# Optimization experiments

Hardware: AMD Instinct MI355X
Metric: run time of the kernel (lower is better)

## Reference

```python
import jax, jax.numpy as jnp
import numpy as np

B, S, D = 4, 2048, 1024
H = 2 * D          # hidden_dim = 2*n_embd
A = H // 16        # adapt_dim = 128
E = 8              # num_experts
K = 2              # top-k within group
GS = 4             # group_size
G = E // GS        # num_groups


def _ln(x, g, b, eps=1e-5):
    m = x.mean(-1, keepdims=True)
    v = x.var(-1, keepdims=True)
    return (x - m) / jnp.sqrt(v + eps) * g + b


def setup_inputs() -> dict:
    key = jax.random.key(0)
    ks = jax.random.split(key, 12)
    s = 1.0 / np.sqrt(D)       # shared MLP init scale
    sa = s * 0.01              # adapt layers init scale
    se = 0.01 / np.sqrt(A)     # expert adapter init scale
    f32 = jnp.float32
    return {
        "x": jax.random.normal(ks[0], (B, S, D), f32),
        "W_up": jax.random.normal(ks[1], (H, D), f32) * s,
        "W_gate": jax.random.normal(ks[2], (H, D), f32) * s,
        "W_down": jax.random.normal(ks[3], (D, H), f32) * s,
        "W_pre": jax.random.normal(ks[4], (A, D), f32) * sa,
        "W_post": jax.random.normal(ks[5], (A, H), f32) * sa,
        "g_an": jnp.ones((A,), f32),
        "b_an": jnp.zeros((A,), f32),
        "W_aproj": jax.random.normal(ks[6], (H, A), f32) * sa,
        "W_eadapt": jax.random.normal(ks[7], (E, A, A), f32) * se,
        "g_e": jnp.ones((E, A), f32),
        "b_e": jnp.zeros((E, A), f32),
        "W_eproj": jax.random.normal(ks[8], (H, A), f32) * se,
        "W_oproj": jax.random.normal(ks[9], (D, H), f32) * se,
        "W_rg": jax.random.normal(ks[10], (G, D), f32) * 0.001,
        "W_re": jax.random.normal(ks[11], (GS, D), f32) * 0.001,
    }


def reference(x, W_up, W_gate, W_down, W_pre, W_post, g_an, b_an, W_aproj,
              W_eadapt, g_e, b_e, W_eproj, W_oproj, W_rg, W_re):
    Bs, Ss, Ds = x.shape
    N = Bs * Ss
    xf = x.reshape(N, Ds)

    # ---- HierarchicalRouter ----
    gl = xf @ W_rg.T                                   # [N, G]
    gp = jax.nn.softmax(gl, axis=-1)
    gw = gp.max(axis=-1)                               # top-1 group weight
    gi = gp.argmax(axis=-1)                            # top-1 group index
    ll = xf @ W_re.T                                   # [N, GS]
    lp = jax.nn.softmax(ll, axis=-1)
    lw, li = jax.lax.top_k(lp, K)                      # [N, K]
    eidx = gi[:, None] * GS + li                       # global expert ids
    lw = lw / (lw.sum(-1, keepdims=True) + 1e-7)
    fw = gw[:, None] * lw                              # final weights [N, K]
    dispatch = jnp.zeros((N, E), x.dtype).at[jnp.arange(N)[:, None], eidx].set(fw)
    load = dispatch.sum(0)
    target = load.sum() / E
    load_balance_loss = jnp.mean((load - target) ** 2)
    z_loss = jnp.mean(gl ** 2) + jnp.mean(ll ** 2)
    router_loss = 0.001 * (load_balance_loss + z_loss)

    # ---- SharedExpertMLP ----
    up = x @ W_up.T                                    # [B, S, H]
    gate = x @ W_gate.T
    hidden = jax.nn.silu(gate) * up
    pre = x @ W_pre.T                                  # [B, S, A]
    a_in = _ln(pre, g_an, b_an)
    a_out = _ln(hidden @ W_post.T, g_an, b_an)
    aw = jax.nn.silu(jnp.clip(jnp.einsum('bsa,bta->bst', a_in, a_out), -5.0, 5.0))
    adapt = jnp.einsum('bst,bta->bsa', aw, a_in) @ W_aproj.T  # [B, S, H]
    hidden = hidden + 0.1 * adapt
    shared = hidden @ W_down.T                         # [B, S, D]

    # ---- ExpertGroup (vectorized gather/MLP/scatter) ----
    # sum_i w_i * (shared + 0.1*contrib_i) = shared*sum(w) + 0.1*sum_i w_i*contrib_i
    w = dispatch.reshape(Bs, Ss, E)                    # dispatch weights
    he = jnp.einsum('bsa,eca->ebsc', pre, W_eadapt)    # [E, B, S, A]
    he = _ln(he, g_e[:, None, None, :], b_e[:, None, None, :])
    wh = jnp.einsum('ebsa,bse->bsa', he, w)            # weighted combine at adapt_dim
    contrib = (wh @ W_eproj.T) @ W_oproj.T             # [B, S, D]
    out = shared * w.sum(-1, keepdims=True) + 0.1 * contrib
    return out, router_loss
```

## Files before the change

kernel.cpp:

```cpp
#include <hip/hip_runtime.h>
#include <hip/hip_bf16.h>

typedef unsigned short u16;
typedef short bf16x8 __attribute__((ext_vector_type(8)));
typedef float f32x4 __attribute__((ext_vector_type(4)));

#define N_TOK 8192
#define DIM   1024
#define HID   2048
#define ADIM  128
#define SEQ   2048
#define LDP   2304

__device__ __forceinline__ u16 f2bf_bits(float f){
  unsigned u = __float_as_uint(f);
  unsigned r = (u + 0x7fffu + ((u >> 16) & 1u)) >> 16;
  return (u16)r;
}
__device__ __forceinline__ float bf2f(u16 v){ return __uint_as_float((unsigned)v << 16); }
__device__ __forceinline__ float siluf(float x){ return x / (1.f + __expf(-x)); }

__device__ __forceinline__ void gload16(const void* g, void* l){
  __builtin_amdgcn_global_load_lds((const __attribute__((address_space(1))) void*)g,
                                   (__attribute__((address_space(3))) void*)l, 16, 0, 0);
}


__global__ void __launch_bounds__(512, 2)
gemm_gu256(const u16* __restrict__ X, const u16* __restrict__ Wgu,
           const float* __restrict__ sumw, u16* __restrict__ hidP)
{
  extern __shared__ u16 lds[];
  const int tid = threadIdx.x, w = tid >> 6, lane = tid & 63;
  const int wm = w >> 2, wn = w & 3;
  const int xcd = blockIdx.x & 7, lloc = blockIdx.x >> 3;
  const int bm = (xcd >> 1) * 8 + (lloc & 7);
  const int bn = (xcd & 1) * 8 + (lloc >> 3);
  const long brow = (long)bm * 256, bcol = (long)bn * 256;
  const int frow = lane & 15;
  const int fks = ((lane >> 4) * 8) ^ (((lane >> 1) & 3) << 3);
  const int srow = lane >> 2;
  const int sslot = (((lane & 3) ^ ((lane >> 3) & 3)) * 8);

  f32x4 acc[8][4];
  #pragma unroll
  for (int m = 0; m < 8; m++)
    #pragma unroll
    for (int n = 0; n < 4; n++)
      #pragma unroll
      for (int i = 0; i < 4; i++) acc[m][n][i] = 0.f;

  auto stage = [&](const u16* __restrict__ gbase, long row0, int kt, int kh,
                   int p, int regoff) {
    #pragma unroll
    for (int i = 0; i < 2; i++) {
      const int r = (i * 8 + w) * 16 + srow;
      const u16* g = gbase + (row0 + r) * 1024 + kt * 64 + kh * 32 + sslot;
      u16* l = &lds[p * 32768 + regoff + kh * 8192 + (i * 8 + w) * 512];
      gload16(g, l);
    }
  };

#define AFRAG(mf, kss) (*(const bf16x8*)&lds[p*32768 + (kss)*8192 + (wm*128 + (mf)*16 + frow)*32 + fks])
#define BFRAG(nf, kss) (*(const bf16x8*)&lds[p*32768 + 16384 + (kss)*8192 + (wn*64 + (nf)*16 + frow)*32 + fks])

  stage(X, brow, 0, 0, 0, 0);
  stage(Wgu, bcol, 0, 0, 0, 16384);
  stage(X, brow, 0, 1, 0, 0);
  stage(Wgu, bcol, 0, 1, 0, 16384);
  asm volatile("s_waitcnt vmcnt(4)" ::: "memory");
  __builtin_amdgcn_s_barrier();

  for (int kt = 0; kt < 16; ++kt) {
    const int p = kt & 1, pn = p ^ 1;
    const int ktn = (kt < 15) ? kt + 1 : 15;
    bf16x8 b[4], a[4];

    #pragma unroll
    for (int n = 0; n < 4; n++) b[n] = BFRAG(n, 0);
    #pragma unroll
    for (int m = 0; m < 4; m++) a[m] = AFRAG(m, 0);
    stage(X, brow, ktn, 0, pn, 0);
    __builtin_amdgcn_s_barrier();
    asm volatile("s_waitcnt lgkmcnt(0)" ::: "memory");
    __builtin_amdgcn_sched_barrier(0);
    __builtin_amdgcn_s_setprio(1);
    #pragma unroll
    for (int m = 0; m < 4; m++)
      #pragma unroll
      for (int n = 0; n < 4; n++)
        acc[m][n] = __builtin_amdgcn_mfma_f32_16x16x32_bf16(a[m], b[n], acc[m][n], 0, 0, 0);
    __builtin_amdgcn_s_setprio(0);
    __builtin_amdgcn_s_barrier();

    #pragma unroll
    for (int m = 0; m < 4; m++) a[m] = AFRAG(m + 4, 0);
    stage(Wgu, bcol, ktn, 0, pn, 16384);
    __builtin_amdgcn_s_barrier();
    asm volatile("s_waitcnt lgkmcnt(0)" ::: "memory");
    __builtin_amdgcn_sched_barrier(0);
    __builtin_amdgcn_s_setprio(1);
    #pragma unroll
    for (int m = 0; m < 4; m++)
      #pragma unroll
      for (int n = 0; n < 4; n++)
        acc[m + 4][n] = __builtin_amdgcn_mfma_f32_16x16x32_bf16(a[m], b[n], acc[m + 4][n], 0, 0, 0);
    __builtin_amdgcn_s_setprio(0);
    asm volatile("s_waitcnt vmcnt(4)" ::: "memory");
    __builtin_amdgcn_s_barrier();

    #pragma unroll
    for (int n = 0; n < 4; n++) b[n] = BFRAG(n, 1);
    #pragma unroll
    for (int m = 0; m < 4; m++) a[m] = AFRAG(m, 1);
    stage(X, brow, ktn, 1, pn, 0);
    __builtin_amdgcn_s_barrier();
    asm volatile("s_waitcnt lgkmcnt(0)" ::: "memory");
    __builtin_amdgcn_sched_barrier(0);
    __builtin_amdgcn_s_setprio(1);
    #pragma unroll
    for (int m = 0; m < 4; m++)
      #pragma unroll
      for (int n = 0; n < 4; n++)
        acc[m][n] = __builtin_amdgcn_mfma_f32_16x16x32_bf16(a[m], b[n], acc[m][n], 0, 0, 0);
    __builtin_amdgcn_s_setprio(0);
    __builtin_amdgcn_s_barrier();

    #pragma unroll
    for (int m = 0; m < 4; m++) a[m] = AFRAG(m + 4, 1);
    stage(Wgu, bcol, ktn, 1, pn, 16384);
    __builtin_amdgcn_s_barrier();
    asm volatile("s_waitcnt lgkmcnt(0)" ::: "memory");
    __builtin_amdgcn_sched_barrier(0);
    __builtin_amdgcn_s_setprio(1);
    #pragma unroll
    for (int m = 0; m < 4; m++)
      #pragma unroll
      for (int n = 0; n < 4; n++)
        acc[m + 4][n] = __builtin_amdgcn_mfma_f32_16x16x32_bf16(a[m], b[n], acc[m + 4][n], 0, 0, 0);
    __builtin_amdgcn_s_setprio(0);
    asm volatile("s_waitcnt vmcnt(4)" ::: "memory");
    __builtin_amdgcn_s_barrier();
  }
#undef AFRAG
#undef BFRAG

  #pragma unroll
  for (int mf = 0; mf < 8; mf++)
    #pragma unroll
    for (int i = 0; i < 4; i++) {
      const long r = brow + wm * 128 + mf * 16 + (lane >> 4) * 4 + i;
      const float sw = sumw[r];
      #pragma unroll
      for (int q = 0; q < 2; q++) {
        const float g = acc[mf][2 * q][i], u = acc[mf][2 * q + 1][i];
        const int hcol = (bn * 8 + wn * 2 + q) * 16 + (lane & 15);
        hidP[r * LDP + hcol] = f2bf_bits(sw * (siluf(g) * u));
      }
    }
}

enum { EPI_BF16 = 0, EPI_SILU = 2 };

template<int EPI>
__global__ void __launch_bounds__(256, 2)
gemm_bt(const u16* __restrict__ Ag, const u16* __restrict__ Bg, int K, int lda, int ldb,
        long sAz, long sBz, long sOz, u16* __restrict__ bout, int ldo, int col0)
{
  __shared__ u16 lA[128 * 32];
  __shared__ u16 lB[128 * 32];
  const int tid = threadIdx.x, wave = tid >> 6, lane = tid & 63;
  const long brow = (long)blockIdx.y * 128, bcol = (long)blockIdx.x * 128;
  const u16* A = Ag + (long)blockIdx.z * sAz + brow * lda;
  const u16* B = Bg + (long)blockIdx.z * sBz + bcol * ldb;
  const int wr = (wave >> 1) * 64, wc = (wave & 1) * 64;

  f32x4 acc[4][4];
  #pragma unroll
  for (int m = 0; m < 4; m++)
    #pragma unroll
    for (int n = 0; n < 4; n++)
      #pragma unroll
      for (int i = 0; i < 4; i++) acc[m][n][i] = 0.f;

  const int sr = tid >> 2, sks = ((tid & 3) ^ ((tid >> 3) & 3)) * 8;
  const u16* gA = A + (long)sr * lda + sks;
  const u16* gB = B + (long)sr * ldb + sks;
  const long rA = (long)64 * lda, rB = (long)64 * ldb;
  u16* lA0 = &lA[wave * 512]; u16* lA1 = &lA[2048 + wave * 512];
  u16* lB0 = &lB[wave * 512]; u16* lB1 = &lB[2048 + wave * 512];
  const int frow = lane & 15;
  const int fks = ((lane >> 4) * 8) ^ (((lane >> 1) & 3) << 3);

  for (int kt = 0; kt < K; kt += 32) {
    gload16(gA, lA0); gload16(gA + rA, lA1);
    gload16(gB, lB0); gload16(gB + rB, lB1);
    gA += 32; gB += 32;
    asm volatile("s_waitcnt vmcnt(0)" ::: "memory");
    __syncthreads();
    bf16x8 af[4], bfv[4];
    #pragma unroll
    for (int m = 0; m < 4; m++) af[m] = *(const bf16x8*)&lA[(wr + m * 16 + frow) * 32 + fks];
    #pragma unroll
    for (int n = 0; n < 4; n++) bfv[n] = *(const bf16x8*)&lB[(wc + n * 16 + frow) * 32 + fks];
    #pragma unroll
    for (int m = 0; m < 4; m++)
      #pragma unroll
      for (int n = 0; n < 4; n++)
        acc[m][n] = __builtin_amdgcn_mfma_f32_16x16x32_bf16(af[m], bfv[n], acc[m][n], 0, 0, 0);
    __syncthreads();
  }

  const long r0 = brow + wr + ((lane >> 4) << 2);
  const long c0 = bcol + wc + (lane & 15);
  u16* O = bout + (long)blockIdx.z * sOz;
  #pragma unroll
  for (int m = 0; m < 4; m++) {
    #pragma unroll
    for (int i = 0; i < 4; i++) {
      long r = r0 + m * 16 + i;
      #pragma unroll
      for (int n = 0; n < 4; n++) {
        long c = c0 + n * 16;
        float v = acc[m][n][i];
        if constexpr (EPI == EPI_BF16) {
          O[r * ldo + col0 + c] = f2bf_bits(v);
        } else {
          v = fminf(5.f, fmaxf(-5.f, v));
          O[r * ldo + c] = f2bf_bits(siluf(v));
        }
      }
    }
  }
}

__global__ void __launch_bounds__(256, 2)
gemm_f32(const u16* __restrict__ Ag, const u16* __restrict__ Bg,
         float* __restrict__ out)
{
  __shared__ u16 lA[128 * 32];
  __shared__ u16 lB[128 * 32];
  const int tid = threadIdx.x, wave = tid >> 6, lane = tid & 63;
  const long brow = (long)blockIdx.y * 128, bcol = (long)blockIdx.x * 128;
  const int wr = (wave >> 1) * 64, wc = (wave & 1) * 64;

  f32x4 acc[4][4];
  #pragma unroll
  for (int m = 0; m < 4; m++)
    #pragma unroll
    for (int n = 0; n < 4; n++)
      #pragma unroll
      for (int i = 0; i < 4; i++) acc[m][n][i] = 0.f;

  const int sr = tid >> 2, sks = ((tid & 3) ^ ((tid >> 3) & 3)) * 8;
  const u16* gA = Ag + brow * LDP + (long)sr * LDP + sks;
  const u16* gB = Bg + bcol * LDP + (long)sr * LDP + sks;
  const long rA = (long)64 * LDP, rB = (long)64 * LDP;
  u16* lA0 = &lA[wave * 512]; u16* lA1 = &lA[2048 + wave * 512];
  u16* lB0 = &lB[wave * 512]; u16* lB1 = &lB[2048 + wave * 512];
  const int frow = lane & 15;
  const int fks = ((lane >> 4) * 8) ^ (((lane >> 1) & 3) << 3);

  for (int kt = 0; kt < LDP; kt += 32) {
    gload16(gA, lA0); gload16(gA + rA, lA1);
    gload16(gB, lB0); gload16(gB + rB, lB1);
    gA += 32; gB += 32;
    asm volatile("s_waitcnt vmcnt(0)" ::: "memory");
    __syncthreads();
    bf16x8 af[4], bfv[4];
    #pragma unroll
    for (int m = 0; m < 4; m++) af[m] = *(const bf16x8*)&lA[(wr + m * 16 + frow) * 32 + fks];
    #pragma unroll
    for (int n = 0; n < 4; n++) bfv[n] = *(const bf16x8*)&lB[(wc + n * 16 + frow) * 32 + fks];
    #pragma unroll
    for (int m = 0; m < 4; m++)
      #pragma unroll
      for (int n = 0; n < 4; n++)
        acc[m][n] = __builtin_amdgcn_mfma_f32_16x16x32_bf16(af[m], bfv[n], acc[m][n], 0, 0, 0);
    __syncthreads();
  }

  const long r0 = brow + wr + ((lane >> 4) << 2);
  const long c0 = bcol + wc + (lane & 15);
  #pragma unroll
  for (int m = 0; m < 4; m++)
    #pragma unroll
    for (int i = 0; i < 4; i++) {
      long r = r0 + m * 16 + i;
      #pragma unroll
      for (int n = 0; n < 4; n++)
        out[r * DIM + c0 + n * 16] = acc[m][n][i];
    }
}

__global__ void __launch_bounds__(256, 2)
gemm_split(const u16* __restrict__ Ag, const u16* __restrict__ Bg, int Ksub, int nsplit,
           int lda, int ldb, long sAz, long sBz, float* __restrict__ part)
{
  __shared__ u16 lA[128 * 32];
  __shared__ u16 lB[128 * 32];
  const int tid = threadIdx.x, wave = tid >> 6, lane = tid & 63;
  const int z = blockIdx.z, batch = z / nsplit, split = z % nsplit;
  const long brow = (long)blockIdx.y * 128;
  const int Mrows = gridDim.y * 128;
  const u16* A = Ag + (long)batch * sAz + brow * lda + (long)split * Ksub;
  const u16* B = Bg + (long)batch * sBz + (long)split * Ksub;
  const int wr = (wave >> 1) * 64, wc = (wave & 1) * 64;

  f32x4 acc[4][4];
  #pragma unroll
  for (int m = 0; m < 4; m++)
    #pragma unroll
    for (int n = 0; n < 4; n++)
      #pragma unroll
      for (int i = 0; i < 4; i++) acc[m][n][i] = 0.f;

  const int sr = tid >> 2, sks = ((tid & 3) ^ ((tid >> 3) & 3)) * 8;
  const u16* gA = A + (long)sr * lda + sks;
  const u16* gB = B + (long)sr * ldb + sks;
  const long rA = (long)64 * lda, rB = (long)64 * ldb;
  u16* lA0 = &lA[wave * 512]; u16* lA1 = &lA[2048 + wave * 512];
  u16* lB0 = &lB[wave * 512]; u16* lB1 = &lB[2048 + wave * 512];
  const int frow = lane & 15;
  const int fks = ((lane >> 4) * 8) ^ (((lane >> 1) & 3) << 3);

  for (int kt = 0; kt < Ksub; kt += 32) {
    gload16(gA, lA0); gload16(gA + rA, lA1);
    gload16(gB, lB0); gload16(gB + rB, lB1);
    gA += 32; gB += 32;
    asm volatile("s_waitcnt vmcnt(0)" ::: "memory");
    __syncthreads();
    bf16x8 af[4], bfv[4];
    #pragma unroll
    for (int m = 0; m < 4; m++) af[m] = *(const bf16x8*)&lA[(wr + m * 16 + frow) * 32 + fks];
    #pragma unroll
    for (int n = 0; n < 4; n++) bfv[n] = *(const bf16x8*)&lB[(wc + n * 16 + frow) * 32 + fks];
    #pragma unroll
    for (int m = 0; m < 4; m++)
      #pragma unroll
      for (int n = 0; n < 4; n++)
        acc[m][n] = __builtin_amdgcn_mfma_f32_16x16x32_bf16(af[m], bfv[n], acc[m][n], 0, 0, 0);
    __syncthreads();
  }

  float* po = part + (long)z * Mrows * 128;
  const long rr = brow + wr + ((lane >> 4) << 2);
  const int cc = wc + (lane & 15);
  #pragma unroll
  for (int m = 0; m < 4; m++)
    #pragma unroll
    for (int i = 0; i < 4; i++) {
      long r = rr + m * 16 + i;
      #pragma unroll
      for (int n = 0; n < 4; n++)
        po[r * 128 + cc + n * 16] = acc[m][n][i];
    }
}

__global__ void wprep(const float* __restrict__ Wg, const float* __restrict__ Wu,
                      const float* __restrict__ Wd, const float* __restrict__ Wo,
                      const float* __restrict__ Wpost, const float* __restrict__ Wpre,
                      const float* __restrict__ Wead,
                      u16* __restrict__ Wgu, u16* __restrict__ WdQ,
                      u16* __restrict__ Wob, u16* __restrict__ Wpostb,
                      u16* __restrict__ Wpreb, u16* __restrict__ Weadb)
{
  long i = ((long)blockIdx.x * 256 + threadIdx.x) * 8;
  const float* s; u16* d; long so, doff;
  if (i < 4194304) {
    long j = i;
    long rp = j >> 10, c = j & 1023;
    long i32 = rp >> 5, wi = rp & 31;
    s = (wi < 16) ? Wg : Wu;
    so = (i32 * 16 + (wi & 15)) * 1024 + c;
    d = Wgu; doff = j;
  } else if (i < 6291456) {
    long j = i - 4194304;
    long r = j >> 11, c = j & 2047;
    s = Wd; so = j;
    d = WdQ; doff = r * LDP + c;
  } else if (i < 8388608) { s = Wo;    so = i - 6291456; d = Wob;    doff = so; }
  else if (i < 8650752)   { s = Wpost; so = i - 8388608; d = Wpostb; doff = so; }
  else if (i < 8781824)   { s = Wpre;  so = i - 8650752; d = Wpreb;  doff = so; }
  else                    { s = Wead;  so = i - 8781824; d = Weadb;  doff = so; }
  float4 v0 = *(const float4*)(s + so), v1 = *(const float4*)(s + so + 4);
  ushort4 p, q;
  p.x = f2bf_bits(v0.x); p.y = f2bf_bits(v0.y); p.z = f2bf_bits(v0.z); p.w = f2bf_bits(v0.w);
  q.x = f2bf_bits(v1.x); q.y = f2bf_bits(v1.y); q.z = f2bf_bits(v1.z); q.w = f2bf_bits(v1.w);
  *(ushort4*)(d + doff) = p;
  *(ushort4*)(d + doff + 4) = q;
}

__global__ void cvt_t2(const float* __restrict__ Wa, const float* __restrict__ We,
                       u16* __restrict__ Ta, u16* __restrict__ Te)
{
  int bid = blockIdx.x;
  const float* src = (bid < 1024) ? Wa : We;
  u16* dst = (bid < 1024) ? Ta : Te;
  int idx = (bid & 1023) * 256 + threadIdx.x;
  int c = idx >> 11, r = idx & 2047;
  dst[idx] = f2bf_bits(src[(long)r * 128 + c]);
}

__global__ void reduce_q(const float* __restrict__ part, u16* __restrict__ WdQ)
{
  int idx = blockIdx.x * 256 + threadIdx.x;
  int r = idx >> 8, c = idx & 255;
  const float* p = part + ((c < 128) ? 0 : 524288) + (long)r * 128 + (c & 127);
  float a = p[0] + p[131072] + p[262144] + p[393216];
  WdQ[(long)r * LDP + 2048 + c] = f2bf_bits(a);
}

__global__ void __launch_bounds__(256)
ln_rows_part(const float* __restrict__ part, int nsplit,
             const float* __restrict__ g, const float* __restrict__ b,
             const float* __restrict__ sumw,
             u16* __restrict__ out, u16* __restrict__ outT, u16* __restrict__ rawout)
{
  int wave = threadIdx.x >> 6, lane = threadIdx.x & 63;
  long n = (long)blockIdx.x * 4 + wave;
  long base = n * 128;
  float x0 = 0.f, x1 = 0.f;
  for (int s = 0; s < nsplit; s++) {
    x0 += part[(long)s * (N_TOK * ADIM) + base + lane];
    x1 += part[(long)s * (N_TOK * ADIM) + base + 64 + lane];
  }
  if (sumw) { float inv = 1.f / sumw[n]; x0 *= inv; x1 *= inv; }
  float s2 = x0 + x1, q = x0 * x0 + x1 * x1;
  #pragma unroll
  for (int o = 32; o; o >>= 1) { s2 += __shfl_xor(s2, o); q += __shfl_xor(q, o); }
  float m = s2 * (1.f / 128.f);
  float var = q * (1.f / 128.f) - m * m;
  float inv = rsqrtf(var + 1e-5f);
  float y0 = (x0 - m) * inv * g[lane] + b[lane];
  float y1 = (x1 - m) * inv * g[lane + 64] + b[lane + 64];
  out[base + lane] = f2bf_bits(y0);
  out[base + 64 + lane] = f2bf_bits(y1);
  if (outT) {
    long bb = n >> 11, ss = n & 2047;
    outT[(bb * 128 + lane) * 2048 + ss] = f2bf_bits(y0);
    outT[(bb * 128 + lane + 64) * 2048 + ss] = f2bf_bits(y1);
  }
  if (rawout) {
    rawout[base + lane] = f2bf_bits(x0);
    rawout[base + 64 + lane] = f2bf_bits(x1);
  }
}

__global__ void reduce_part_p1(const float* __restrict__ part,
                               const float* __restrict__ sumw, u16* __restrict__ hidP)
{
  int idx = blockIdx.x * 256 + threadIdx.x;
  int n = idx >> 5, c4 = (idx & 31) * 4;
  int batch = n >> 11, r = n & 2047;
  float4 a = {0.f, 0.f, 0.f, 0.f};
  #pragma unroll
  for (int s = 0; s < 4; s++) {
    float4 v = *(const float4*)(part + (((long)(batch * 4 + s) * 2048 + r) << 7) + c4);
    a.x += v.x; a.y += v.y; a.z += v.z; a.w += v.w;
  }
  float rs = 0.1f * sumw[n];
  ushort4 o;
  o.x = f2bf_bits(rs * a.x); o.y = f2bf_bits(rs * a.y);
  o.z = f2bf_bits(rs * a.z); o.w = f2bf_bits(rs * a.w);
  *(ushort4*)(hidP + (long)n * LDP + 2048 + c4) = o;
}

__global__ void __launch_bounds__(256)
router_kernel(const float* __restrict__ x, const float* __restrict__ Wrg,
              const float* __restrict__ Wre, float* __restrict__ sumw,
              float* __restrict__ fwv, int* __restrict__ eidxv,
              float* __restrict__ stats, u16* __restrict__ xb)
{
  __shared__ float lst[10];
  if (threadIdx.x < 10) lst[threadIdx.x] = 0.f;
  __syncthreads();
  const int wave = threadIdx.x >> 6, lane = threadIdx.x & 63;
  const float4* wg0 = (const float4*)Wrg;
  const float4* wg1 = (const float4*)(Wrg + 1024);
  const float4* we0 = (const float4*)Wre;
  const float4* we1 = (const float4*)(Wre + 1024);
  const float4* we2 = (const float4*)(Wre + 2048);
  const float4* we3 = (const float4*)(Wre + 3072);

  for (int t = 0; t < 4; t++) {
    const long n = (long)blockIdx.x * 16 + wave * 4 + t;
    const float4* xr = (const float4*)(x + n * 1024);
    float d0 = 0, d1 = 0, t0 = 0, t1 = 0, t2 = 0, t3 = 0;
    #pragma unroll
    for (int j = 0; j < 4; j++) {
      int id = j * 64 + lane;
      float4 xv = xr[id];
      ushort4 xc;
      xc.x = f2bf_bits(xv.x); xc.y = f2bf_bits(xv.y);
      xc.z = f2bf_bits(xv.z); xc.w = f2bf_bits(xv.w);
      *(ushort4*)(xb + n * 1024 + id * 4) = xc;
      float4 a;
      a = wg0[id]; d0 += xv.x * a.x + xv.y * a.y + xv.z * a.z + xv.w * a.w;
      a = wg1[id]; d1 += xv.x * a.x + xv.y * a.y + xv.z * a.z + xv.w * a.w;
      a = we0[id]; t0 += xv.x * a.x + xv.y * a.y + xv.z * a.z + xv.w * a.w;
      a = we1[id]; t1 += xv.x * a.x + xv.y * a.y + xv.z * a.z + xv.w * a.w;
      a = we2[id]; t2 += xv.x * a.x + xv.y * a.y + xv.z * a.z + xv.w * a.w;
      a = we3[id]; t3 += xv.x * a.x + xv.y * a.y + xv.z * a.z + xv.w * a.w;
    }
    #pragma unroll
    for (int o = 32; o; o >>= 1) {
      d0 += __shfl_xor(d0, o); d1 += __shfl_xor(d1, o);
      t0 += __shfl_xor(t0, o); t1 += __shfl_xor(t1, o);
      t2 += __shfl_xor(t2, o); t3 += __shfl_xor(t3, o);
    }
    if (lane == 0) {
      float mg = fmaxf(d0, d1);
      float e0 = __expf(d0 - mg), e1 = __expf(d1 - mg);
      float invg = 1.f / (e0 + e1);
      float p0 = e0 * invg, p1 = e1 * invg;
      int gi = (d1 > d0) ? 1 : 0;
      float gw = fmaxf(p0, p1);
      float l[4] = {t0, t1, t2, t3};
      float ml = fmaxf(fmaxf(l[0], l[1]), fmaxf(l[2], l[3]));
      float p[4]; float su = 0;
      #pragma unroll
      for (int i = 0; i < 4; i++) { p[i] = __expf(l[i] - ml); su += p[i]; }
      float isu = 1.f / su;
      #pragma unroll
      for (int i = 0; i < 4; i++) p[i] *= isu;
      int i1 = 0;
      #pragma unroll
      for (int i = 1; i < 4; i++) if (p[i] > p[i1]) i1 = i;
      int i2 = (i1 == 0) ? 1 : 0;
      #pragma unroll
      for (int i = 0; i < 4; i++) if (i != i1 && p[i] > p[i2]) i2 = i;
      float s2 = p[i1] + p[i2];
      float invs = 1.f / (s2 + 1e-7f);
      float f1 = gw * p[i1] * invs, f2 = gw * p[i2] * invs;
      int ea = gi * 4 + i1, eb = gi * 4 + i2;
      sumw[n] = f1 + f2;
      fwv[2 * n] = f1; fwv[2 * n + 1] = f2;
      eidxv[2 * n] = ea; eidxv[2 * n + 1] = eb;
      atomicAdd(&lst[ea], f1);
      atomicAdd(&lst[eb], f2);
      atomicAdd(&lst[8], d0 * d0 + d1 * d1);
      atomicAdd(&lst[9], t0 * t0 + t1 * t1 + t2 * t2 + t3 * t3);
    }
  }
  __syncthreads();
  if (threadIdx.x < 10) atomicAdd(&stats[threadIdx.x], lst[threadIdx.x]);
}

__global__ void init_stats(float* stats){ if (threadIdx.x < 16) stats[threadIdx.x] = 0.f; }

__global__ void finalize_loss(const float* __restrict__ stats, float* __restrict__ out)
{
  float tot = 0;
  #pragma unroll
  for (int e = 0; e < 8; e++) tot += stats[e];
  float target = tot * 0.125f;
  float lb = 0;
  #pragma unroll
  for (int e = 0; e < 8; e++) { float d = stats[e] - target; lb += d * d; }
  lb *= 0.125f;
  float z = stats[8] * (1.f / (8192.f * 2.f)) + stats[9] * (1.f / (8192.f * 4.f));
  out[0] = 0.001f * (lb + z);
}

__global__ void __launch_bounds__(256)
ln_combine(const u16* __restrict__ he, const int* __restrict__ eidxv,
           const float* __restrict__ fwv, const float* __restrict__ g_e,
           const float* __restrict__ b_e, u16* __restrict__ hidP)
{
  const int wave = threadIdx.x >> 6, lane = threadIdx.x & 63;
  const long n = (long)blockIdx.x * 4 + wave;
  float o0 = 0.f, o1 = 0.f;
  #pragma unroll
  for (int k = 0; k < 2; k++) {
    const int e = eidxv[2 * n + k];
    const float w = fwv[2 * n + k];
    const u16* row = he + ((long)e * N_TOK + n) * 128;
    float h0 = bf2f(row[lane]), h1 = bf2f(row[lane + 64]);
    float s = h0 + h1, q = h0 * h0 + h1 * h1;
    #pragma unroll
    for (int o = 32; o; o >>= 1) { s += __shfl_xor(s, o); q += __shfl_xor(q, o); }
    float m = s * (1.f / 128.f);
    float var = q * (1.f / 128.f) - m * m;
    float inv = rsqrtf(var + 1e-5f);
    o0 += w * ((h0 - m) * inv * g_e[e * 128 + lane] + b_e[e * 128 + lane]);
    o1 += w * ((h1 - m) * inv * g_e[e * 128 + lane + 64] + b_e[e * 128 + lane + 64]);
  }
  hidP[n * LDP + 2176 + lane] = f2bf_bits(0.1f * o0);
  hidP[n * LDP + 2176 + 64 + lane] = f2bf_bits(0.1f * o1);
}

extern "C" void kernel_launch(void* const* d_in, const int* in_sizes, int n_in,
                              void* d_out, int out_size, void* d_ws, size_t ws_size,
                              hipStream_t stream)
{
  (void)in_sizes; (void)n_in; (void)out_size; (void)ws_size;
  const float* x       = (const float*)d_in[0];
  const float* W_up    = (const float*)d_in[1];
  const float* W_gate  = (const float*)d_in[2];
  const float* W_down  = (const float*)d_in[3];
  const float* W_pre   = (const float*)d_in[4];
  const float* W_post  = (const float*)d_in[5];
  const float* g_an    = (const float*)d_in[6];
  const float* b_an    = (const float*)d_in[7];
  const float* W_aproj = (const float*)d_in[8];
  const float* W_ead   = (const float*)d_in[9];
  const float* g_e     = (const float*)d_in[10];
  const float* b_e     = (const float*)d_in[11];
  const float* W_eproj = (const float*)d_in[12];
  const float* W_oproj = (const float*)d_in[13];
  const float* W_rg    = (const float*)d_in[14];
  const float* W_re    = (const float*)d_in[15];
  float* out = (float*)d_out;

  char* base = (char*)d_ws; size_t off = 0;
  auto alloc = [&](size_t bytes) -> void* {
    void* p = base + off; off = (off + bytes + 255) & ~(size_t)255; return p;
  };
  u16*   xb     = (u16*)  alloc((size_t)N_TOK * DIM * 2);
  u16*   Wgu    = (u16*)  alloc((size_t)2 * HID * DIM * 2);
  u16*   WdQ    = (u16*)  alloc((size_t)DIM * LDP * 2);
  u16*   Wob    = (u16*)  alloc((size_t)DIM * HID * 2);
  u16*   Wpostb = (u16*)  alloc((size_t)ADIM * HID * 2);
  u16*   Wpreb  = (u16*)  alloc((size_t)ADIM * DIM * 2);
  u16*   WaTb   = (u16*)  alloc((size_t)ADIM * HID * 2);
  u16*   WeTb   = (u16*)  alloc((size_t)ADIM * HID * 2);
  u16*   Weadb  = (u16*)  alloc((size_t)8 * ADIM * ADIM * 2);
  u16*   hidP   = (u16*)  alloc((size_t)N_TOK * LDP * 2);
  u16*   heb    = (u16*)  alloc((size_t)8 * N_TOK * ADIM * 2);
  float* part   = (float*)heb;
  u16*   preb   = (u16*)  alloc((size_t)N_TOK * ADIM * 2);
  u16*   a_in   = (u16*)  alloc((size_t)N_TOK * ADIM * 2);
  u16*   a_inT  = (u16*)  alloc((size_t)N_TOK * ADIM * 2);
  u16*   a_out  = (u16*)  alloc((size_t)N_TOK * ADIM * 2);
  float* sumw   = (float*)alloc((size_t)N_TOK * 4);
  float* fwv    = (float*)alloc((size_t)N_TOK * 2 * 4);
  int*   eidxv  = (int*)  alloc((size_t)N_TOK * 2 * 4);
  float* stats  = (float*)alloc(64);
  u16* aw = (u16*)d_out;

  hipFuncSetAttribute((const void*)gemm_gu256,
                      hipFuncAttributeMaxDynamicSharedMemorySize, 131072);

  init_stats<<<1, 64, 0, stream>>>(stats);
  router_kernel<<<512, 256, 0, stream>>>(x, W_rg, W_re, sumw, fwv, eidxv, stats, xb);

  wprep<<<4352, 256, 0, stream>>>(W_gate, W_up, W_down, W_oproj, W_post, W_pre, W_ead,
                                  Wgu, WdQ, Wob, Wpostb, Wpreb, Weadb);
  cvt_t2<<<2048, 256, 0, stream>>>(W_aproj, W_eproj, WaTb, WeTb);

  gemm_split<<<dim3(1, 8, 4), 256, 0, stream>>>(WdQ, WaTb, 512, 4, LDP, HID, 0, 0, part);
  gemm_split<<<dim3(1, 8, 4), 256, 0, stream>>>(Wob, WeTb, 512, 4, HID, HID, 0, 0,
      part + 524288);
  reduce_q<<<1024, 256, 0, stream>>>(part, WdQ);

  gemm_gu256<<<512, 512, 131072, stream>>>(xb, Wgu, sumw, hidP);

  gemm_split<<<dim3(1, 64, 4), 256, 0, stream>>>(xb, Wpreb, 256, 4, DIM, DIM, 0, 0, part);
  ln_rows_part<<<2048, 256, 0, stream>>>(part, 4, g_an, b_an, nullptr, a_in, a_inT, preb);

  gemm_bt<EPI_BF16><<<dim3(1, 64, 8), 256, 0, stream>>>(preb, Weadb, ADIM, ADIM, ADIM,
      0, (long)ADIM * ADIM, (long)N_TOK * ADIM, heb, ADIM, 0);
  ln_combine<<<2048, 256, 0, stream>>>(heb, eidxv, fwv, g_e, b_e, hidP);

  gemm_split<<<dim3(1, 64, 4), 256, 0, stream>>>(hidP, Wpostb, 512, 4, LDP, HID, 0, 0, part);
  ln_rows_part<<<2048, 256, 0, stream>>>(part, 4, g_an, b_an, sumw, a_out, nullptr, nullptr);

  gemm_bt<EPI_SILU><<<dim3(16, 16, 4), 256, 0, stream>>>(a_in, a_out, ADIM, ADIM, ADIM,
      (long)SEQ * ADIM, (long)SEQ * ADIM, (long)SEQ * SEQ, aw, SEQ, 0);

  gemm_split<<<dim3(1, 16, 16), 256, 0, stream>>>(aw, a_inT, 512, 4, SEQ, SEQ,
      (long)SEQ * SEQ, (long)ADIM * SEQ, part);
  reduce_part_p1<<<1024, 256, 0, stream>>>(part, sumw, hidP);

  gemm_f32<<<dim3(8, 64, 1), 256, 0, stream>>>(hidP, WdQ, out);

  finalize_loss<<<1, 1, 0, stream>>>(stats, out + (size_t)N_TOK * DIM);
}
```

Baseline: 286.9 us.

## Fuse prep kernels, merge weight-fold GEMMs, and stagger LDS waits in gate/up GEMM

```diff
diff --git a/kernel.cpp b/kernel.cpp
--- a/kernel.cpp
+++ b/kernel.cpp
@@ -25,6 +25,7 @@
                                    (__attribute__((address_space(3))) void*)l, 16, 0, 0);
 }
 
+#define SB0() __builtin_amdgcn_sched_barrier(0)
 
 __global__ void __launch_bounds__(512, 2)
 gemm_gu256(const u16* __restrict__ X, const u16* __restrict__ Wgu,
@@ -76,68 +77,112 @@
     const int ktn = (kt < 15) ? kt + 1 : 15;
     bf16x8 b[4], a[4];
 
-    #pragma unroll
-    for (int n = 0; n < 4; n++) b[n] = BFRAG(n, 0);
-    #pragma unroll
-    for (int m = 0; m < 4; m++) a[m] = AFRAG(m, 0);
+    a[0] = AFRAG(0, 0);
+    b[0] = BFRAG(0, 0); b[1] = BFRAG(1, 0); b[2] = BFRAG(2, 0); b[3] = BFRAG(3, 0);
+    SB0();
+    a[1] = AFRAG(1, 0); SB0();
+    a[2] = AFRAG(2, 0); SB0();
+    a[3] = AFRAG(3, 0);
     stage(X, brow, ktn, 0, pn, 0);
     __builtin_amdgcn_s_barrier();
-    asm volatile("s_waitcnt lgkmcnt(0)" ::: "memory");
-    __builtin_amdgcn_sched_barrier(0);
+    asm volatile("s_waitcnt lgkmcnt(3)" ::: "memory"); SB0();
     __builtin_amdgcn_s_setprio(1);
     #pragma unroll
-    for (int m = 0; m < 4; m++)
-      #pragma unroll
-      for (int n = 0; n < 4; n++)
-        acc[m][n] = __builtin_amdgcn_mfma_f32_16x16x32_bf16(a[m], b[n], acc[m][n], 0, 0, 0);
+    for (int n = 0; n < 4; n++)
+      acc[0][n] = __builtin_amdgcn_mfma_f32_16x16x32_bf16(a[0], b[n], acc[0][n], 0, 0, 0);
+    asm volatile("s_waitcnt lgkmcnt(2)" ::: "memory"); SB0();
+    #pragma unroll
+    for (int n = 0; n < 4; n++)
+      acc[1][n] = __builtin_amdgcn_mfma_f32_16x16x32_bf16(a[1], b[n], acc[1][n], 0, 0, 0);
+    asm volatile("s_waitcnt lgkmcnt(1)" ::: "memory"); SB0();
+    #pragma unroll
+    for (int n = 0; n < 4; n++)
+      acc[2][n] = __builtin_amdgcn_mfma_f32_16x16x32_bf16(a[2], b[n], acc[2][n], 0, 0, 0);
+    asm volatile("s_waitcnt lgkmcnt(0)" ::: "memory"); SB0();
+    #pragma unroll
+    for (int n = 0; n < 4; n++)
+      acc[3][n] = __builtin_amdgcn_mfma_f32_16x16x32_bf16(a[3], b[n], acc[3][n], 0, 0, 0);
     __builtin_amdgcn_s_setprio(0);
     __builtin_amdgcn_s_barrier();
 
-    #pragma unroll
-    for (int m = 0; m < 4; m++) a[m] = AFRAG(m + 4, 0);
+    a[0] = AFRAG(4, 0); SB0();
+    a[1] = AFRAG(5, 0); SB0();
+    a[2] = AFRAG(6, 0); SB0();
+    a[3] = AFRAG(7, 0);
     stage(Wgu, bcol, ktn, 0, pn, 16384);
     __builtin_amdgcn_s_barrier();
-    asm volatile("s_waitcnt lgkmcnt(0)" ::: "memory");
-    __builtin_amdgcn_sched_barrier(0);
+    asm volatile("s_waitcnt lgkmcnt(3)" ::: "memory"); SB0();
     __builtin_amdgcn_s_setprio(1);
     #pragma unroll
-    for (int m = 0; m < 4; m++)
-      #pragma unroll
-      for (int n = 0; n < 4; n++)
-        acc[m + 4][n] = __builtin_amdgcn_mfma_f32_16x16x32_bf16(a[m], b[n], acc[m + 4][n], 0, 0, 0);
+    for (int n = 0; n < 4; n++)
+      acc[4][n] = __builtin_amdgcn_mfma_f32_16x16x32_bf16(a[0], b[n], acc[4][n], 0, 0, 0);
+    asm volatile("s_waitcnt lgkmcnt(2)" ::: "memory"); SB0();
+    #pragma unroll
+    for (int n = 0; n < 4; n++)
+      acc[5][n] = __builtin_amdgcn_mfma_f32_16x16x32_bf16(a[1], b[n], acc[5][n], 0, 0, 0);
+    asm volatile("s_waitcnt lgkmcnt(1)" ::: "memory"); SB0();
+    #pragma unroll
+    for (int n = 0; n < 4; n++)
+      acc[6][n] = __builtin_amdgcn_mfma_f32_16x16x32_bf16(a[2], b[n], acc[6][n], 0, 0, 0);
+    asm volatile("s_waitcnt lgkmcnt(0)" ::: "memory"); SB0();
+    #pragma unroll
+    for (int n = 0; n < 4; n++)
+      acc[7][n] = __builtin_amdgcn_mfma_f32_16x16x32_bf16(a[3], b[n], acc[7][n], 0, 0, 0);
     __builtin_amdgcn_s_setprio(0);
     asm volatile("s_waitcnt vmcnt(4)" ::: "memory");
     __builtin_amdgcn_s_barrier();
 
-    #pragma unroll
-    for (int n = 0; n < 4; n++) b[n] = BFRAG(n, 1);
-    #pragma unroll
-    for (int m = 0; m < 4; m++) a[m] = AFRAG(m, 1);
+    a[0] = AFRAG(0, 1);
+    b[0] = BFRAG(0, 1); b[1] = BFRAG(1, 1); b[2] = BFRAG(2, 1); b[3] = BFRAG(3, 1);
+    SB0();
+    a[1] = AFRAG(1, 1); SB0();
+    a[2] = AFRAG(2, 1); SB0();
+    a[3] = AFRAG(3, 1);
     stage(X, brow, ktn, 1, pn, 0);
     __builtin_amdgcn_s_barrier();
-    asm volatile("s_waitcnt lgkmcnt(0)" ::: "memory");
-    __builtin_amdgcn_sched_barrier(0);
+    asm volatile("s_waitcnt lgkmcnt(3)" ::: "memory"); SB0();
     __builtin_amdgcn_s_setprio(1);
     #pragma unroll
-    for (int m = 0; m < 4; m++)
-      #pragma unroll
-      for (int n = 0; n < 4; n++)
-        acc[m][n] = __builtin_amdgcn_mfma_f32_16x16x32_bf16(a[m], b[n], acc[m][n], 0, 0, 0);
+    for (int n = 0; n < 4; n++)
+      acc[0][n] = __builtin_amdgcn_mfma_f32_16x16x32_bf16(a[0], b[n], acc[0][n], 0, 0, 0);
+    asm volatile("s_waitcnt lgkmcnt(2)" ::: "memory"); SB0();
+    #pragma unroll
+    for (int n = 0; n < 4; n++)
+      acc[1][n] = __builtin_amdgcn_mfma_f32_16x16x32_bf16(a[1], b[n], acc[1][n], 0, 0, 0);
+    asm volatile("s_waitcnt lgkmcnt(1)" ::: "memory"); SB0();
+    #pragma unroll
+    for (int n = 0; n < 4; n++)
+      acc[2][n] = __builtin_amdgcn_mfma_f32_16x16x32_bf16(a[2], b[n], acc[2][n], 0, 0, 0);
+    asm volatile("s_waitcnt lgkmcnt(0)" ::: "memory"); SB0();
+    #pragma unroll
+    for (int n = 0; n < 4; n++)
+      acc[3][n] = __builtin_amdgcn_mfma_f32_16x16x32_bf16(a[3], b[n], acc[3][n], 0, 0, 0);
     __builtin_amdgcn_s_setprio(0);
     __builtin_amdgcn_s_barrier();
 
-    #pragma unroll
-    for (int m = 0; m < 4; m++) a[m] = AFRAG(m + 4, 1);
+    a[0] = AFRAG(4, 1); SB0();
+    a[1] = AFRAG(5, 1); SB0();
+    a[2] = AFRAG(6, 1); SB0();
+    a[3] = AFRAG(7, 1);
     stage(Wgu, bcol, ktn, 1, pn, 16384);
     __builtin_amdgcn_s_barrier();
-    asm volatile("s_waitcnt lgkmcnt(0)" ::: "memory");
-    __builtin_amdgcn_sched_barrier(0);
+    asm volatile("s_waitcnt lgkmcnt(3)" ::: "memory"); SB0();
     __builtin_amdgcn_s_setprio(1);
     #pragma unroll
-    for (int m = 0; m < 4; m++)
-      #pragma unroll
-      for (int n = 0; n < 4; n++)
-        acc[m + 4][n] = __builtin_amdgcn_mfma_f32_16x16x32_bf16(a[m], b[n], acc[m + 4][n], 0, 0, 0);
+    for (int n = 0; n < 4; n++)
+      acc[4][n] = __builtin_amdgcn_mfma_f32_16x16x32_bf16(a[0], b[n], acc[4][n], 0, 0, 0);
+    asm volatile("s_waitcnt lgkmcnt(2)" ::: "memory"); SB0();
+    #pragma unroll
+    for (int n = 0; n < 4; n++)
+      acc[5][n] = __builtin_amdgcn_mfma_f32_16x16x32_bf16(a[1], b[n], acc[5][n], 0, 0, 0);
+    asm volatile("s_waitcnt lgkmcnt(1)" ::: "memory"); SB0();
+    #pragma unroll
+    for (int n = 0; n < 4; n++)
+      acc[6][n] = __builtin_amdgcn_mfma_f32_16x16x32_bf16(a[2], b[n], acc[6][n], 0, 0, 0);
+    asm volatile("s_waitcnt lgkmcnt(0)" ::: "memory"); SB0();
+    #pragma unroll
+    for (int n = 0; n < 4; n++)
+      acc[7][n] = __builtin_amdgcn_mfma_f32_16x16x32_bf16(a[3], b[n], acc[7][n], 0, 0, 0);
     __builtin_amdgcn_s_setprio(0);
     asm volatile("s_waitcnt vmcnt(4)" ::: "memory");
     __builtin_amdgcn_s_barrier();
@@ -357,49 +402,192 @@
     }
 }
 
-__global__ void wprep(const float* __restrict__ Wg, const float* __restrict__ Wu,
-                      const float* __restrict__ Wd, const float* __restrict__ Wo,
-                      const float* __restrict__ Wpost, const float* __restrict__ Wpre,
-                      const float* __restrict__ Wead,
-                      u16* __restrict__ Wgu, u16* __restrict__ WdQ,
-                      u16* __restrict__ Wob, u16* __restrict__ Wpostb,
-                      u16* __restrict__ Wpreb, u16* __restrict__ Weadb)
-{
-  long i = ((long)blockIdx.x * 256 + threadIdx.x) * 8;
-  const float* s; u16* d; long so, doff;
-  if (i < 4194304) {
-    long j = i;
-    long rp = j >> 10, c = j & 1023;
-    long i32 = rp >> 5, wi = rp & 31;
-    s = (wi < 16) ? Wg : Wu;
-    so = (i32 * 16 + (wi & 15)) * 1024 + c;
-    d = Wgu; doff = j;
-  } else if (i < 6291456) {
-    long j = i - 4194304;
-    long r = j >> 11, c = j & 2047;
-    s = Wd; so = j;
-    d = WdQ; doff = r * LDP + c;
-  } else if (i < 8388608) { s = Wo;    so = i - 6291456; d = Wob;    doff = so; }
-  else if (i < 8650752)   { s = Wpost; so = i - 8388608; d = Wpostb; doff = so; }
-  else if (i < 8781824)   { s = Wpre;  so = i - 8650752; d = Wpreb;  doff = so; }
-  else                    { s = Wead;  so = i - 8781824; d = Weadb;  doff = so; }
-  float4 v0 = *(const float4*)(s + so), v1 = *(const float4*)(s + so + 4);
-  ushort4 p, q;
-  p.x = f2bf_bits(v0.x); p.y = f2bf_bits(v0.y); p.z = f2bf_bits(v0.z); p.w = f2bf_bits(v0.w);
-  q.x = f2bf_bits(v1.x); q.y = f2bf_bits(v1.y); q.z = f2bf_bits(v1.z); q.w = f2bf_bits(v1.w);
-  *(ushort4*)(d + doff) = p;
-  *(ushort4*)(d + doff + 4) = q;
-}
-
-__global__ void cvt_t2(const float* __restrict__ Wa, const float* __restrict__ We,
-                       u16* __restrict__ Ta, u16* __restrict__ Te)
-{
-  int bid = blockIdx.x;
-  const float* src = (bid < 1024) ? Wa : We;
-  u16* dst = (bid < 1024) ? Ta : Te;
-  int idx = (bid & 1023) * 256 + threadIdx.x;
-  int c = idx >> 11, r = idx & 2047;
-  dst[idx] = f2bf_bits(src[(long)r * 128 + c]);
+__global__ void __launch_bounds__(256, 2)
+gemm_split_q(const u16* __restrict__ A0, const u16* __restrict__ B0, int lda0,
+             const u16* __restrict__ A1, const u16* __restrict__ B1, int lda1,
+             float* __restrict__ part)
+{
+  __shared__ u16 lA[128 * 32];
+  __shared__ u16 lB[128 * 32];
+  const int tid = threadIdx.x, wave = tid >> 6, lane = tid & 63;
+  const int z = blockIdx.z, sel = z >> 2, split = z & 3;
+  const long brow = (long)blockIdx.y * 128;
+  const int lda = sel ? lda1 : lda0;
+  const u16* A = (sel ? A1 : A0) + brow * lda + (long)split * 512;
+  const u16* B = (sel ? B1 : B0) + (long)split * 512;
+
+  const int wr = (wave >> 1) * 64, wc = (wave & 1) * 64;
+  f32x4 acc[4][4];
+  #pragma unroll
+  for (int m = 0; m < 4; m++)
+    #pragma unroll
+    for (int n = 0; n < 4; n++)
+      #pragma unroll
+      for (int i = 0; i < 4; i++) acc[m][n][i] = 0.f;
+
+  const int sr = tid >> 2, sks = ((tid & 3) ^ ((tid >> 3) & 3)) * 8;
+  const u16* gA = A + (long)sr * lda + sks;
+  const u16* gB = B + (long)sr * HID + sks;
+  const long rA = (long)64 * lda, rB = (long)64 * HID;
+  u16* lA0 = &lA[wave * 512]; u16* lA1 = &lA[2048 + wave * 512];
+  u16* lB0 = &lB[wave * 512]; u16* lB1 = &lB[2048 + wave * 512];
+  const int frow = lane & 15;
+  const int fks = ((lane >> 4) * 8) ^ (((lane >> 1) & 3) << 3);
+
+  for (int kt = 0; kt < 512; kt += 32) {
+    gload16(gA, lA0); gload16(gA + rA, lA1);
+    gload16(gB, lB0); gload16(gB + rB, lB1);
+    gA += 32; gB += 32;
+    asm volatile("s_waitcnt vmcnt(0)" ::: "memory");
+    __syncthreads();
+    bf16x8 af[4], bfv[4];
+    #pragma unroll
+    for (int m = 0; m < 4; m++) af[m] = *(const bf16x8*)&lA[(wr + m * 16 + frow) * 32 + fks];
+    #pragma unroll
+    for (int n = 0; n < 4; n++) bfv[n] = *(const bf16x8*)&lB[(wc + n * 16 + frow) * 32 + fks];
+    #pragma unroll
+    for (int m = 0; m < 4; m++)
+      #pragma unroll
+      for (int n = 0; n < 4; n++)
+        acc[m][n] = __builtin_amdgcn_mfma_f32_16x16x32_bf16(af[m], bfv[n], acc[m][n], 0, 0, 0);
+    __syncthreads();
+  }
+
+  float* po = part + (long)z * 131072;
+  const long rr = brow + wr + ((lane >> 4) << 2);
+  const int cc = wc + (lane & 15);
+  #pragma unroll
+  for (int m = 0; m < 4; m++)
+    #pragma unroll
+    for (int i = 0; i < 4; i++) {
+      long r = rr + m * 16 + i;
+      #pragma unroll
+      for (int n = 0; n < 4; n++)
+        po[r * 128 + cc + n * 16] = acc[m][n][i];
+    }
+}
+
+__global__ void __launch_bounds__(256)
+prep_all(const float* __restrict__ x, const float* __restrict__ Wrg,
+         const float* __restrict__ Wre, float* __restrict__ sumw,
+         float* __restrict__ fwv, int* __restrict__ eidxv,
+         float* __restrict__ stats, u16* __restrict__ xb,
+         const float* __restrict__ Wg, const float* __restrict__ Wu,
+         const float* __restrict__ Wd, const float* __restrict__ Wo,
+         const float* __restrict__ Wpost, const float* __restrict__ Wpre,
+         const float* __restrict__ Wead,
+         u16* __restrict__ Wgu, u16* __restrict__ WdQ,
+         u16* __restrict__ Wob, u16* __restrict__ Wpostb,
+         u16* __restrict__ Wpreb, u16* __restrict__ Weadb,
+         const float* __restrict__ Wa, const float* __restrict__ We,
+         u16* __restrict__ Ta, u16* __restrict__ Te)
+{
+  __shared__ float lst[10];
+  const int blk = blockIdx.x;
+  if (blk < 512) {
+    if (threadIdx.x < 10) lst[threadIdx.x] = 0.f;
+    __syncthreads();
+    const int wave = threadIdx.x >> 6, lane = threadIdx.x & 63;
+    const float4* wg0 = (const float4*)Wrg;
+    const float4* wg1 = (const float4*)(Wrg + 1024);
+    const float4* we0 = (const float4*)Wre;
+    const float4* we1 = (const float4*)(Wre + 1024);
+    const float4* we2 = (const float4*)(Wre + 2048);
+    const float4* we3 = (const float4*)(Wre + 3072);
+    for (int t = 0; t < 4; t++) {
+      const long n = (long)blk * 16 + wave * 4 + t;
+      const float4* xr = (const float4*)(x + n * 1024);
+      float d0 = 0, d1 = 0, t0 = 0, t1 = 0, t2 = 0, t3 = 0;
+      #pragma unroll
+      for (int j = 0; j < 4; j++) {
+        int id = j * 64 + lane;
+        float4 xv = xr[id];
+        ushort4 xc;
+        xc.x = f2bf_bits(xv.x); xc.y = f2bf_bits(xv.y);
+        xc.z = f2bf_bits(xv.z); xc.w = f2bf_bits(xv.w);
+        *(ushort4*)(xb + n * 1024 + id * 4) = xc;
+        float4 a;
+        a = wg0[id]; d0 += xv.x * a.x + xv.y * a.y + xv.z * a.z + xv.w * a.w;
+        a = wg1[id]; d1 += xv.x * a.x + xv.y * a.y + xv.z * a.z + xv.w * a.w;
+        a = we0[id]; t0 += xv.x * a.x + xv.y * a.y + xv.z * a.z + xv.w * a.w;
+        a = we1[id]; t1 += xv.x * a.x + xv.y * a.y + xv.z * a.z + xv.w * a.w;
+        a = we2[id]; t2 += xv.x * a.x + xv.y * a.y + xv.z * a.z + xv.w * a.w;
+        a = we3[id]; t3 += xv.x * a.x + xv.y * a.y + xv.z * a.z + xv.w * a.w;
+      }
+      #pragma unroll
+      for (int o = 32; o; o >>= 1) {
+        d0 += __shfl_xor(d0, o); d1 += __shfl_xor(d1, o);
+        t0 += __shfl_xor(t0, o); t1 += __shfl_xor(t1, o);
+        t2 += __shfl_xor(t2, o); t3 += __shfl_xor(t3, o);
+      }
+      if (lane == 0) {
+        float mg = fmaxf(d0, d1);
+        float e0 = __expf(d0 - mg), e1 = __expf(d1 - mg);
+        float invg = 1.f / (e0 + e1);
+        float p0 = e0 * invg, p1 = e1 * invg;
+        int gi = (d1 > d0) ? 1 : 0;
+        float gw = fmaxf(p0, p1);
+        float l[4] = {t0, t1, t2, t3};
+        float ml = fmaxf(fmaxf(l[0], l[1]), fmaxf(l[2], l[3]));
+        float p[4]; float su = 0;
+        #pragma unroll
+        for (int i = 0; i < 4; i++) { p[i] = __expf(l[i] - ml); su += p[i]; }
+        float isu = 1.f / su;
+        #pragma unroll
+        for (int i = 0; i < 4; i++) p[i] *= isu;
+        int i1 = 0;
+        #pragma unroll
+        for (int i = 1; i < 4; i++) if (p[i] > p[i1]) i1 = i;
+        int i2 = (i1 == 0) ? 1 : 0;
+        #pragma unroll
+        for (int i = 0; i < 4; i++) if (i != i1 && p[i] > p[i2]) i2 = i;
+        float s2 = p[i1] + p[i2];
+        float invs = 1.f / (s2 + 1e-7f);
+        float f1 = gw * p[i1] * invs, f2 = gw * p[i2] * invs;
+        int ea = gi * 4 + i1, eb = gi * 4 + i2;
+        sumw[n] = f1 + f2;
+        fwv[2 * n] = f1; fwv[2 * n + 1] = f2;
+        eidxv[2 * n] = ea; eidxv[2 * n + 1] = eb;
+        atomicAdd(&lst[ea], f1);
+        atomicAdd(&lst[eb], f2);
+        atomicAdd(&lst[8], d0 * d0 + d1 * d1);
+        atomicAdd(&lst[9], t0 * t0 + t1 * t1 + t2 * t2 + t3 * t3);
+      }
+    }
+    __syncthreads();
+    if (threadIdx.x < 10) atomicAdd(&stats[threadIdx.x], lst[threadIdx.x]);
+  } else if (blk < 4864) {
+    long i = ((long)(blk - 512) * 256 + threadIdx.x) * 8;
+    const float* s; u16* d; long so, doff;
+    if (i < 4194304) {
+      long rp = i >> 10, c = i & 1023;
+      long i32 = rp >> 5, wi = rp & 31;
+      s = (wi < 16) ? Wg : Wu;
+      so = (i32 * 16 + (wi & 15)) * 1024 + c;
+      d = Wgu; doff = i;
+    } else if (i < 6291456) {
+      long j = i - 4194304;
+      long r = j >> 11, c = j & 2047;
+      s = Wd; so = j;
+      d = WdQ; doff = r * LDP + c;
+    } else if (i < 8388608) { s = Wo;    so = i - 6291456; d = Wob;    doff = so; }
+    else if (i < 8650752)   { s = Wpost; so = i - 8388608; d = Wpostb; doff = so; }
+    else if (i < 8781824)   { s = Wpre;  so = i - 8650752; d = Wpreb;  doff = so; }
+    else                    { s = Wead;  so = i - 8781824; d = Weadb;  doff = so; }
+    float4 v0 = *(const float4*)(s + so), v1 = *(const float4*)(s + so + 4);
+    ushort4 p, q;
+    p.x = f2bf_bits(v0.x); p.y = f2bf_bits(v0.y); p.z = f2bf_bits(v0.z); p.w = f2bf_bits(v0.w);
+    q.x = f2bf_bits(v1.x); q.y = f2bf_bits(v1.y); q.z = f2bf_bits(v1.z); q.w = f2bf_bits(v1.w);
+    *(ushort4*)(d + doff) = p;
+    *(ushort4*)(d + doff + 4) = q;
+  } else {
+    int bid = blk - 4864;
+    const float* src = (bid < 1024) ? Wa : We;
+    u16* dst = (bid < 1024) ? Ta : Te;
+    int idx = (bid & 1023) * 256 + threadIdx.x;
+    int c = idx >> 11, r = idx & 2047;
+    dst[idx] = f2bf_bits(src[(long)r * 128 + c]);
+  }
 }
 
 __global__ void reduce_q(const float* __restrict__ part, u16* __restrict__ WdQ)
@@ -464,87 +652,6 @@
   o.x = f2bf_bits(rs * a.x); o.y = f2bf_bits(rs * a.y);
   o.z = f2bf_bits(rs * a.z); o.w = f2bf_bits(rs * a.w);
   *(ushort4*)(hidP + (long)n * LDP + 2048 + c4) = o;
-}
-
-__global__ void __launch_bounds__(256)
-router_kernel(const float* __restrict__ x, const float* __restrict__ Wrg,
-              const float* __restrict__ Wre, float* __restrict__ sumw,
-              float* __restrict__ fwv, int* __restrict__ eidxv,
-              float* __restrict__ stats, u16* __restrict__ xb)
-{
-  __shared__ float lst[10];
-  if (threadIdx.x < 10) lst[threadIdx.x] = 0.f;
-  __syncthreads();
-  const int wave = threadIdx.x >> 6, lane = threadIdx.x & 63;
-  const float4* wg0 = (const float4*)Wrg;
-  const float4* wg1 = (const float4*)(Wrg + 1024);
-  const float4* we0 = (const float4*)Wre;
-  const float4* we1 = (const float4*)(Wre + 1024);
-  const float4* we2 = (const float4*)(Wre + 2048);
-  const float4* we3 = (const float4*)(Wre + 3072);
-
-  for (int t = 0; t < 4; t++) {
-    const long n = (long)blockIdx.x * 16 + wave * 4 + t;
-    const float4* xr = (const float4*)(x + n * 1024);
-    float d0 = 0, d1 = 0, t0 = 0, t1 = 0, t2 = 0, t3 = 0;
-    #pragma unroll
-    for (int j = 0; j < 4; j++) {
-      int id = j * 64 + lane;
-      float4 xv = xr[id];
-      ushort4 xc;
-      xc.x = f2bf_bits(xv.x); xc.y = f2bf_bits(xv.y);
-      xc.z = f2bf_bits(xv.z); xc.w = f2bf_bits(xv.w);
-      *(ushort4*)(xb + n * 1024 + id * 4) = xc;
-      float4 a;
-      a = wg0[id]; d0 += xv.x * a.x + xv.y * a.y + xv.z * a.z + xv.w * a.w;
-      a = wg1[id]; d1 += xv.x * a.x + xv.y * a.y + xv.z * a.z + xv.w * a.w;
-      a = we0[id]; t0 += xv.x * a.x + xv.y * a.y + xv.z * a.z + xv.w * a.w;
-      a = we1[id]; t1 += xv.x * a.x + xv.y * a.y + xv.z * a.z + xv.w * a.w;
-      a = we2[id]; t2 += xv.x * a.x + xv.y * a.y + xv.z * a.z + xv.w * a.w;
-      a = we3[id]; t3 += xv.x * a.x + xv.y * a.y + xv.z * a.z + xv.w * a.w;
-    }
-    #pragma unroll
-    for (int o = 32; o; o >>= 1) {
-      d0 += __shfl_xor(d0, o); d1 += __shfl_xor(d1, o);
-      t0 += __shfl_xor(t0, o); t1 += __shfl_xor(t1, o);
-      t2 += __shfl_xor(t2, o); t3 += __shfl_xor(t3, o);
-    }
-    if (lane == 0) {
-      float mg = fmaxf(d0, d1);
-      float e0 = __expf(d0 - mg), e1 = __expf(d1 - mg);
-      float invg = 1.f / (e0 + e1);
-      float p0 = e0 * invg, p1 = e1 * invg;
-      int gi = (d1 > d0) ? 1 : 0;
-      float gw = fmaxf(p0, p1);
-      float l[4] = {t0, t1, t2, t3};
-      float ml = fmaxf(fmaxf(l[0], l[1]), fmaxf(l[2], l[3]));
-      float p[4]; float su = 0;
-      #pragma unroll
-      for (int i = 0; i < 4; i++) { p[i] = __expf(l[i] - ml); su += p[i]; }
-      float isu = 1.f / su;
-      #pragma unroll
-      for (int i = 0; i < 4; i++) p[i] *= isu;
-      int i1 = 0;
-      #pragma unroll
-      for (int i = 1; i < 4; i++) if (p[i] > p[i1]) i1 = i;
-      int i2 = (i1 == 0) ? 1 : 0;
-      #pragma unroll
-      for (int i = 0; i < 4; i++) if (i != i1 && p[i] > p[i2]) i2 = i;
-      float s2 = p[i1] + p[i2];
-      float invs = 1.f / (s2 + 1e-7f);
-      float f1 = gw * p[i1] * invs, f2 = gw * p[i2] * invs;
-      int ea = gi * 4 + i1, eb = gi * 4 + i2;
-      sumw[n] = f1 + f2;
-      fwv[2 * n] = f1; fwv[2 * n + 1] = f2;
-      eidxv[2 * n] = ea; eidxv[2 * n + 1] = eb;
-      atomicAdd(&lst[ea], f1);
-      atomicAdd(&lst[eb], f2);
-      atomicAdd(&lst[8], d0 * d0 + d1 * d1);
-      atomicAdd(&lst[9], t0 * t0 + t1 * t1 + t2 * t2 + t3 * t3);
-    }
-  }
-  __syncthreads();
-  if (threadIdx.x < 10) atomicAdd(&stats[threadIdx.x], lst[threadIdx.x]);
 }
 
 __global__ void init_stats(float* stats){ if (threadIdx.x < 16) stats[threadIdx.x] = 0.f; }
@@ -643,15 +750,13 @@
                       hipFuncAttributeMaxDynamicSharedMemorySize, 131072);
 
   init_stats<<<1, 64, 0, stream>>>(stats);
-  router_kernel<<<512, 256, 0, stream>>>(x, W_rg, W_re, sumw, fwv, eidxv, stats, xb);
-
-  wprep<<<4352, 256, 0, stream>>>(W_gate, W_up, W_down, W_oproj, W_post, W_pre, W_ead,
-                                  Wgu, WdQ, Wob, Wpostb, Wpreb, Weadb);
-  cvt_t2<<<2048, 256, 0, stream>>>(W_aproj, W_eproj, WaTb, WeTb);
-
-  gemm_split<<<dim3(1, 8, 4), 256, 0, stream>>>(WdQ, WaTb, 512, 4, LDP, HID, 0, 0, part);
-  gemm_split<<<dim3(1, 8, 4), 256, 0, stream>>>(Wob, WeTb, 512, 4, HID, HID, 0, 0,
-      part + 524288);
+
+  prep_all<<<6912, 256, 0, stream>>>(x, W_rg, W_re, sumw, fwv, eidxv, stats, xb,
+                                     W_gate, W_up, W_down, W_oproj, W_post, W_pre,
+                                     W_ead, Wgu, WdQ, Wob, Wpostb, Wpreb, Weadb,
+                                     W_aproj, W_eproj, WaTb, WeTb);
+
+  gemm_split_q<<<dim3(1, 8, 8), 256, 0, stream>>>(WdQ, WaTb, LDP, Wob, WeTb, HID, part);
   reduce_q<<<1024, 256, 0, stream>>>(part, WdQ);
 
   gemm_gu256<<<512, 512, 131072, stream>>>(xb, Wgu, sumw, hidP);
```

Result: faster. 269.9 us (-5.9%).
